# Optimization experiments

Measured on AMD Instinct MI355X. Metric: run time of the kernel, lower is better.

The kernel has to match this reference:

```python
import jax, jax.numpy as jnp
import numpy as np

N_NODES = 150000  # num_users + num_items
EMB_DIM = 64
N_EDGES = 4000000


def setup_inputs() -> dict:
    key = jax.random.key(0)
    k1, k2 = jax.random.split(key)
    x = jax.random.normal(k1, (N_NODES, EMB_DIM), dtype=jnp.float32)
    edge_index = jax.random.randint(k2, (2, N_EDGES), 0, N_NODES, dtype=jnp.int64)
    return {"x": x, "edge_index": edge_index}


def _lgconv(x, row, col, w):
    # message: x[row] * w ; aggregate: scatter-add into col
    msg = x[row] * w[:, None]  # [E, D]
    return jax.ops.segment_sum(msg, col, num_segments=N_NODES)


def reference(x, edge_index):
    row, col = edge_index[0], edge_index[1]
    # gcn_norm without self-loops: deg from target index (col)
    deg = jax.ops.segment_sum(jnp.ones(row.shape[0], x.dtype), col,
                              num_segments=N_NODES)
    dis = jnp.where(deg > 0, jax.lax.rsqrt(jnp.maximum(deg, 1.0)), 0.0)
    w = dis[row] * dis[col]  # [E]

    emb0 = x
    emb1 = _lgconv(emb0, row, col, w)
    emb2 = _lgconv(emb1, row, col, w)
    # stack over layer dim then mean == mean of the three layer embeddings
    out = (emb0 + emb1 + emb2) / 3.0
    return out
```

## Files before the change

### kernel.cpp

```cpp
#include <hip/hip_runtime.h>
#include <hip/hip_bf16.h>


#define EMB_DIM 64
#define BUCKET_BITS 9
#define BUCKET_SZ 512
#define EPB 8192
#define NBMAX 512
#define CAP 16384
#define GSTRIDE 16

typedef float f32x4 __attribute__((ext_vector_type(4)));

__device__ __forceinline__ float bf_lo(unsigned int q) { return __uint_as_float(q << 16); }
__device__ __forceinline__ float bf_hi(unsigned int q) { return __uint_as_float(q & 0xffff0000u); }
__device__ __forceinline__ unsigned int f2bf(float f) {
    unsigned int u = __float_as_uint(f);
    return (u + 0x7fffu + ((u >> 16) & 1u)) >> 16;
}

__global__ void fused_scatter(const int* __restrict__ rows,
                              const int* __restrict__ cols,
                              int* __restrict__ gcur,
                              unsigned int* __restrict__ pairs,
                              int E, int NB) {
    __shared__ unsigned int sbuf[EPB];
    __shared__ unsigned short sbkt[EPB];
    __shared__ int lh[NBMAX];
    __shared__ int lexc[NBMAX];
    __shared__ int ldiff[NBMAX];
    __shared__ int lrank[NBMAX];
    __shared__ int wsum[8];
    int blk = blockIdx.x, t = threadIdx.x;
    for (int b = t; b < NBMAX; b += 1024) lh[b] = 0;
    __syncthreads();
    int start = blk * EPB, end = min(start + EPB, E);
    int nloc = end - start;
    int n4 = nloc >> 2;
    int rem = nloc & 3;
    const int4* c4 = (const int4*)(cols + start);
    const int4* r4 = (const int4*)(rows + start);
    int myc[8], myr[8];
#pragma unroll
    for (int j = 0; j < 8; ++j) myc[j] = -1;
#pragma unroll
    for (int j = 0; j < 2; ++j) {
        int i4 = t + j * 1024;
        if (i4 < n4) {
            int4 cc = c4[i4];
            int4 rr = r4[i4];
            myc[4 * j + 0] = cc.x; myr[4 * j + 0] = rr.x;
            myc[4 * j + 1] = cc.y; myr[4 * j + 1] = rr.y;
            myc[4 * j + 2] = cc.z; myr[4 * j + 2] = rr.z;
            myc[4 * j + 3] = cc.w; myr[4 * j + 3] = rr.w;
        }
    }
    int mycT = -1, myrT = 0;
    if (t < rem) {
        mycT = cols[start + (n4 << 2) + t];
        myrT = rows[start + (n4 << 2) + t];
    }
#pragma unroll
    for (int j = 0; j < 8; ++j)
        if (myc[j] >= 0) atomicAdd(&lh[myc[j] >> BUCKET_BITS], 1);
    if (mycT >= 0) atomicAdd(&lh[mycT >> BUCKET_BITS], 1);
    __syncthreads();
    int v = 0, incl = 0;
    if (t < 512) {
        v = lh[t];
        incl = v;
        int lane = t & 63;
#pragma unroll
        for (int off = 1; off < 64; off <<= 1) {
            int u = __shfl_up(incl, off, 64);
            if (lane >= off) incl += u;
        }
        if (lane == 63) wsum[t >> 6] = incl;
    }
    __syncthreads();
    if (t < 8) {
        int s = wsum[t];
        int inc2 = s;
#pragma unroll
        for (int off = 1; off < 8; off <<= 1) {
            int u = __shfl_up(inc2, off, 64);
            if (t >= off) inc2 += u;
        }
        wsum[t] = inc2 - s;
    }
    __syncthreads();
    int myexc = 0;
    if (t < 512) {
        myexc = (incl - v) + wsum[t >> 6];
        lexc[t] = myexc;
    }
    if (t < NB) {
        int c = lh[t];
        int old = c ? atomicAdd(&gcur[t * GSTRIDE], c) : 0;
        ldiff[t] = (t * CAP + old) - myexc;
        lrank[t] = 0;
    }
    __syncthreads();
#pragma unroll
    for (int j = 0; j < 8; ++j) {
        if (myc[j] >= 0) {
            int b = myc[j] >> BUCKET_BITS;
            int rk = atomicAdd(&lrank[b], 1);
            int p = lexc[b] + rk;
            sbuf[p] = (unsigned)myr[j] |
                      ((unsigned)(myc[j] & (BUCKET_SZ - 1)) << 18);
            sbkt[p] = (unsigned short)b;
        }
    }
    if (mycT >= 0) {
        int b = mycT >> BUCKET_BITS;
        int rk = atomicAdd(&lrank[b], 1);
        int p = lexc[b] + rk;
        sbuf[p] = (unsigned)myrT |
                  ((unsigned)(mycT & (BUCKET_SZ - 1)) << 18);
        sbkt[p] = (unsigned short)b;
    }
    __syncthreads();
    for (int p = t; p < nloc; p += 1024) {
        int b = sbkt[p];
        pairs[ldiff[b] + p] = sbuf[p];
    }
}

__global__ void bucket_finalize(const unsigned int* __restrict__ pairs,
                                const int* __restrict__ gcur,
                                int* __restrict__ edata,
                                int* __restrict__ offsets,
                                float* __restrict__ dis,
                                int N, int E, int NB) {
    __shared__ int sbuf[CAP];
    __shared__ int ccnt[BUCKET_SZ];
    __shared__ int cexc[BUCKET_SZ];
    __shared__ int rnk[BUCKET_SZ];
    __shared__ int wsum[16];
    __shared__ int gb_s;
    int b = blockIdx.x, t = threadIdx.x;
    int pbase = b * CAP;
    int cnt = gcur[b * GSTRIDE];

    int part = 0;
    for (int j = t; j < b; j += 1024) part += gcur[j * GSTRIDE];
#pragma unroll
    for (int off = 32; off; off >>= 1) part += __shfl_down(part, off, 64);
    if ((t & 63) == 0) wsum[t >> 6] = part;
    if (t < BUCKET_SZ) ccnt[t] = 0;
    __syncthreads();
    if (t == 0) {
        int g = 0;
#pragma unroll
        for (int w = 0; w < 16; ++w) g += wsum[w];
        gb_s = g;
    }
    for (int i = t; i < cnt; i += 1024)
        atomicAdd(&ccnt[pairs[pbase + i] >> 18], 1);
    __syncthreads();

    int v = 0, incl = 0;
    if (t < 512) {
        v = ccnt[t];
        incl = v;
        int lane = t & 63;
#pragma unroll
        for (int off = 1; off < 64; off <<= 1) {
            int u = __shfl_up(incl, off, 64);
            if (lane >= off) incl += u;
        }
        if (lane == 63) wsum[t >> 6] = incl;
    }
    __syncthreads();
    if (t < 8) {
        int s = wsum[t];
        int inc2 = s;
#pragma unroll
        for (int off = 1; off < 8; off <<= 1) {
            int u = __shfl_up(inc2, off, 64);
            if (t >= off) inc2 += u;
        }
        wsum[t] = inc2 - s;
    }
    __syncthreads();
    if (t < 512) cexc[t] = (incl - v) + wsum[t >> 6];
    if (t < BUCKET_SZ) rnk[t] = 0;
    __syncthreads();

    int base = gb_s;
    int col0 = b << BUCKET_BITS;
    int ncols = min(BUCKET_SZ, N - col0);
    if (t < ncols) {
        int c = ccnt[t];
        offsets[col0 + t] = base + cexc[t];
        dis[col0 + t] = (c > 0) ? rsqrtf((float)c) : 0.0f;
    }
    __syncthreads();
    for (int i = t; i < cnt; i += 1024) {
        unsigned p = pairs[pbase + i];
        int lc = p >> 18;
        int rk = atomicAdd(&rnk[lc], 1);
        sbuf[cexc[lc] + rk] = p & 0x3FFFF;
    }
    __syncthreads();
    for (int i = t; i < cnt; i += 1024)
        edata[base + i] = sbuf[i];
}

__global__ void yb_kernel(const float* __restrict__ x,
                          const float* __restrict__ dis,
                          unsigned short* __restrict__ yb,
                          int* __restrict__ offsets, int N, int E) {
    int tid = blockIdx.x * blockDim.x + threadIdx.x;
    if (tid == 0) offsets[N] = E;
    int nth = gridDim.x * blockDim.x;
    int total = N * 16;
    for (int u = tid; u < total; u += nth) {
        int lr = u >> 4;
        int part = u & 15;
        float d = dis[lr];
        size_t o = (((size_t)lr) << 6) + part * 4;
        float4 vx = *(const float4*)(x + o);
        uint2 w;
        w.x = f2bf(vx.x * d) | (f2bf(vx.y * d) << 16);
        w.y = f2bf(vx.z * d) | (f2bf(vx.w * d) << 16);
        *(uint2*)(yb + o) = w;
    }
}

__device__ __forceinline__ void acc8(float* acc, uint4 q) {
    acc[0] += bf_lo(q.x);
    acc[1] += bf_hi(q.x);
    acc[2] += bf_lo(q.y);
    acc[3] += bf_hi(q.y);
    acc[4] += bf_lo(q.z);
    acc[5] += bf_hi(q.z);
    acc[6] += bf_lo(q.w);
    acc[7] += bf_hi(q.w);
}

template <bool FINAL>
__global__ void agg_kernel(const unsigned short* __restrict__ embb,
                           const int* __restrict__ edata,
                           const int* __restrict__ offsets,
                           const float* __restrict__ dis,
                           const float* __restrict__ x,
                           unsigned short* __restrict__ outb,
                           float* __restrict__ outf,
                           int n) {
    int wave = (blockIdx.x * blockDim.x + threadIdx.x) >> 6;
    int lane = threadIdx.x & 63;
    int sub = lane >> 3;
    int dest = (wave << 3) + sub;
    if (dest >= n) return;
    int dimo = (lane & 7) * 8;

    int s = offsets[dest];
    int e = offsets[dest + 1];

    float a0[8] = {0, 0, 0, 0, 0, 0, 0, 0};
    float a1[8] = {0, 0, 0, 0, 0, 0, 0, 0};
    const unsigned short* eb = embb + dimo;

    int k = s;
    int kfull = s + ((e - s) & ~7);
    for (; k < kfull; k += 8) {
        int s0 = edata[k];
        int s1 = edata[k + 1];
        int s2 = edata[k + 2];
        int s3 = edata[k + 3];
        int s4 = edata[k + 4];
        int s5 = edata[k + 5];
        int s6 = edata[k + 6];
        int s7 = edata[k + 7];
        uint4 q0 = *(const uint4*)(eb + ((size_t)s0 << 6));
        uint4 q1 = *(const uint4*)(eb + ((size_t)s1 << 6));
        uint4 q2 = *(const uint4*)(eb + ((size_t)s2 << 6));
        uint4 q3 = *(const uint4*)(eb + ((size_t)s3 << 6));
        uint4 q4 = *(const uint4*)(eb + ((size_t)s4 << 6));
        uint4 q5 = *(const uint4*)(eb + ((size_t)s5 << 6));
        uint4 q6 = *(const uint4*)(eb + ((size_t)s6 << 6));
        uint4 q7 = *(const uint4*)(eb + ((size_t)s7 << 6));
        acc8(a0, q0);
        acc8(a1, q1);
        acc8(a0, q2);
        acc8(a1, q3);
        acc8(a0, q4);
        acc8(a1, q5);
        acc8(a0, q6);
        acc8(a1, q7);
    }
    if (k < e) {
        int s0 = edata[k];
        int s1 = (k + 1 < e) ? edata[k + 1] : -1;
        int s2 = (k + 2 < e) ? edata[k + 2] : -1;
        int s3 = (k + 3 < e) ? edata[k + 3] : -1;
        int s4 = (k + 4 < e) ? edata[k + 4] : -1;
        int s5 = (k + 5 < e) ? edata[k + 5] : -1;
        int s6 = (k + 6 < e) ? edata[k + 6] : -1;
        int s7 = (k + 7 < e) ? edata[k + 7] : -1;
        uint4 q0, q1, q2, q3, q4, q5, q6, q7;
        q0 = *(const uint4*)(eb + ((size_t)s0 << 6));
        if (s1 >= 0) q1 = *(const uint4*)(eb + ((size_t)s1 << 6));
        if (s2 >= 0) q2 = *(const uint4*)(eb + ((size_t)s2 << 6));
        if (s3 >= 0) q3 = *(const uint4*)(eb + ((size_t)s3 << 6));
        if (s4 >= 0) q4 = *(const uint4*)(eb + ((size_t)s4 << 6));
        if (s5 >= 0) q5 = *(const uint4*)(eb + ((size_t)s5 << 6));
        if (s6 >= 0) q6 = *(const uint4*)(eb + ((size_t)s6 << 6));
        if (s7 >= 0) q7 = *(const uint4*)(eb + ((size_t)s7 << 6));
        acc8(a0, q0);
        if (s1 >= 0) acc8(a1, q1);
        if (s2 >= 0) acc8(a0, q2);
        if (s3 >= 0) acc8(a1, q3);
        if (s4 >= 0) acc8(a0, q4);
        if (s5 >= 0) acc8(a1, q5);
        if (s6 >= 0) acc8(a0, q6);
        if (s7 >= 0) acc8(a1, q7);
    }

    float acc[8];
#pragma unroll
    for (int j = 0; j < 8; ++j) acc[j] = a0[j] + a1[j];

    float dc = dis[dest];
    size_t o = ((size_t)dest << 6) + dimo;
    if (FINAL) {
        float rd = (dc > 0.0f) ? 1.0f / dc : 0.0f;
        f32x4 xa = __builtin_nontemporal_load((const f32x4*)(x + o));
        f32x4 xc = __builtin_nontemporal_load((const f32x4*)(x + o) + 1);
        uint4 qz = *(const uint4*)(embb + o);
        const float k3 = 1.0f / 3.0f;
        f32x4 r0, r1;
        r0.x = (xa.x + bf_lo(qz.x) * rd + dc * acc[0]) * k3;
        r0.y = (xa.y + bf_hi(qz.x) * rd + dc * acc[1]) * k3;
        r0.z = (xa.z + bf_lo(qz.y) * rd + dc * acc[2]) * k3;
        r0.w = (xa.w + bf_hi(qz.y) * rd + dc * acc[3]) * k3;
        r1.x = (xc.x + bf_lo(qz.z) * rd + dc * acc[4]) * k3;
        r1.y = (xc.y + bf_hi(qz.z) * rd + dc * acc[5]) * k3;
        r1.z = (xc.z + bf_lo(qz.w) * rd + dc * acc[6]) * k3;
        r1.w = (xc.w + bf_hi(qz.w) * rd + dc * acc[7]) * k3;
        __builtin_nontemporal_store(r0, (f32x4*)(outf + o));
        __builtin_nontemporal_store(r1, (f32x4*)(outf + o) + 1);
    } else {
        float zs = dc * dc;
        uint4 q;
        q.x = f2bf(zs * acc[0]) | (f2bf(zs * acc[1]) << 16);
        q.y = f2bf(zs * acc[2]) | (f2bf(zs * acc[3]) << 16);
        q.z = f2bf(zs * acc[4]) | (f2bf(zs * acc[5]) << 16);
        q.w = f2bf(zs * acc[6]) | (f2bf(zs * acc[7]) << 16);
        *(uint4*)(outb + o) = q;
    }
}

extern "C" void kernel_launch(void* const* d_in, const int* in_sizes, int n_in,
                              void* d_out, int out_size, void* d_ws, size_t ws_size,
                              hipStream_t stream) {
    const float* x  = (const float*)d_in[0];
    const int*   ei = (const int*)d_in[1];
    const int E = in_sizes[1] / 2;
    const int N = in_sizes[0] / EMB_DIM;

    const int* rows = ei;
    const int* cols = ei + E;

    const int NB = (N + BUCKET_SZ - 1) >> BUCKET_BITS;
    const int NBLK = (E + EPB - 1) / EPB;

    int*   gcur    = (int*)d_ws;
    float* dis     = (float*)(gcur + 512 * GSTRIDE);
    int*   offsets = (int*)(dis + 150080);
    int*   edata   = offsets + 150080;
    unsigned short* yb = (unsigned short*)(edata + E);
    unsigned short* zb = yb + (size_t)N * EMB_DIM;
    unsigned int* pairs = (unsigned int*)zb;
    float* out = (float*)d_out;

    hipMemsetAsync(gcur, 0, 512 * GSTRIDE * sizeof(int), stream);
    fused_scatter<<<NBLK, 1024, 0, stream>>>(rows, cols, gcur, pairs, E, NB);
    bucket_finalize<<<NB, 1024, 0, stream>>>(pairs, gcur, edata, offsets,
                                             dis, N, E, NB);
    yb_kernel<<<2048, 256, 0, stream>>>(x, dis, yb, offsets, N, E);

    int agg_waves = (N + 7) / 8;
    int agg_blocks = (agg_waves + 3) / 4;
    agg_kernel<false><<<agg_blocks, 256, 0, stream>>>(yb, edata, offsets, dis,
                                                      nullptr, zb, nullptr, N);
    agg_kernel<true><<<agg_blocks, 256, 0, stream>>>(zb, edata, offsets, dis,
                                                     x, nullptr, out, N);
}
```

Baseline: 281.3 us.

## Fuse first aggregation layer into bucket finalize using shared-memory CSR

Degree counting moves into the scatter kernel through global atomics, so the scaled bf16 embeddings can be built before bucket finalization. The bucket finalize kernel then runs the first aggregation layer directly from its shared-memory sorted edge list, which removes one kernel launch and one global read of edata. The pairs buffer now lives in the output buffer, and dis is recomputed from degree counts. The trade-offs are about 4M extra global atomics in the scatter kernel and only 150 blocks of 1024 threads doing the first aggregation, which may cost parallelism.

```diff
diff --git a/kernel.cpp b/kernel.cpp
--- a/kernel.cpp
+++ b/kernel.cpp
@@ -19,9 +19,21 @@
     return (u + 0x7fffu + ((u >> 16) & 1u)) >> 16;
 }
 
+__device__ __forceinline__ void acc8(float* acc, uint4 q) {
+    acc[0] += bf_lo(q.x);
+    acc[1] += bf_hi(q.x);
+    acc[2] += bf_lo(q.y);
+    acc[3] += bf_hi(q.y);
+    acc[4] += bf_lo(q.z);
+    acc[5] += bf_hi(q.z);
+    acc[6] += bf_lo(q.w);
+    acc[7] += bf_hi(q.w);
+}
+
 __global__ void fused_scatter(const int* __restrict__ rows,
                               const int* __restrict__ cols,
                               int* __restrict__ gcur,
+                              int* __restrict__ deg,
                               unsigned int* __restrict__ pairs,
                               int E, int NB) {
     __shared__ unsigned int sbuf[EPB];
@@ -61,9 +73,16 @@
         myrT = rows[start + (n4 << 2) + t];
     }
 #pragma unroll
-    for (int j = 0; j < 8; ++j)
-        if (myc[j] >= 0) atomicAdd(&lh[myc[j] >> BUCKET_BITS], 1);
-    if (mycT >= 0) atomicAdd(&lh[mycT >> BUCKET_BITS], 1);
+    for (int j = 0; j < 8; ++j) {
+        if (myc[j] >= 0) {
+            atomicAdd(&deg[myc[j]], 1);
+            atomicAdd(&lh[myc[j] >> BUCKET_BITS], 1);
+        }
+    }
+    if (mycT >= 0) {
+        atomicAdd(&deg[mycT], 1);
+        atomicAdd(&lh[mycT >> BUCKET_BITS], 1);
+    }
     __syncthreads();
     int v = 0, incl = 0;
     if (t < 512) {
@@ -127,12 +146,36 @@
     }
 }
 
-__global__ void bucket_finalize(const unsigned int* __restrict__ pairs,
-                                const int* __restrict__ gcur,
-                                int* __restrict__ edata,
-                                int* __restrict__ offsets,
-                                float* __restrict__ dis,
-                                int N, int E, int NB) {
+__global__ void yb_kernel(const float* __restrict__ x,
+                          const int* __restrict__ deg,
+                          unsigned short* __restrict__ yb,
+                          int* __restrict__ offsets, int N, int E) {
+    int tid = blockIdx.x * blockDim.x + threadIdx.x;
+    if (tid == 0) offsets[N] = E;
+    int nth = gridDim.x * blockDim.x;
+    int total = N * 16;
+    for (int u = tid; u < total; u += nth) {
+        int lr = u >> 4;
+        int part = u & 15;
+        int dg = deg[lr];
+        float d = (dg > 0) ? rsqrtf((float)dg) : 0.0f;
+        size_t o = (((size_t)lr) << 6) + part * 4;
+        float4 vx = *(const float4*)(x + o);
+        uint2 w;
+        w.x = f2bf(vx.x * d) | (f2bf(vx.y * d) << 16);
+        w.y = f2bf(vx.z * d) | (f2bf(vx.w * d) << 16);
+        *(uint2*)(yb + o) = w;
+    }
+}
+
+__global__ __launch_bounds__(1024)
+void agg1_bucket(const unsigned int* __restrict__ pairs,
+                 const int* __restrict__ gcur,
+                 const unsigned short* __restrict__ yb,
+                 unsigned short* __restrict__ zb,
+                 int* __restrict__ edata,
+                 int* __restrict__ offsets,
+                 int N, int NB) {
     __shared__ int sbuf[CAP];
     __shared__ int ccnt[BUCKET_SZ];
     __shared__ int cexc[BUCKET_SZ];
@@ -184,71 +227,118 @@
         wsum[t] = inc2 - s;
     }
     __syncthreads();
-    if (t < 512) cexc[t] = (incl - v) + wsum[t >> 6];
-    if (t < BUCKET_SZ) rnk[t] = 0;
+    if (t < 512) {
+        int e = (incl - v) + wsum[t >> 6];
+        cexc[t] = e;
+        rnk[t] = e;
+    }
     __syncthreads();
 
     int base = gb_s;
     int col0 = b << BUCKET_BITS;
     int ncols = min(BUCKET_SZ, N - col0);
-    if (t < ncols) {
-        int c = ccnt[t];
-        offsets[col0 + t] = base + cexc[t];
-        dis[col0 + t] = (c > 0) ? rsqrtf((float)c) : 0.0f;
-    }
+    if (t < ncols) offsets[col0 + t] = base + cexc[t];
     __syncthreads();
     for (int i = t; i < cnt; i += 1024) {
         unsigned p = pairs[pbase + i];
         int lc = p >> 18;
         int rk = atomicAdd(&rnk[lc], 1);
-        sbuf[cexc[lc] + rk] = p & 0x3FFFF;
+        sbuf[rk] = p & 0x3FFFF;
     }
     __syncthreads();
     for (int i = t; i < cnt; i += 1024)
         edata[base + i] = sbuf[i];
-}
-
-__global__ void yb_kernel(const float* __restrict__ x,
-                          const float* __restrict__ dis,
-                          unsigned short* __restrict__ yb,
-                          int* __restrict__ offsets, int N, int E) {
-    int tid = blockIdx.x * blockDim.x + threadIdx.x;
-    if (tid == 0) offsets[N] = E;
-    int nth = gridDim.x * blockDim.x;
-    int total = N * 16;
-    for (int u = tid; u < total; u += nth) {
-        int lr = u >> 4;
-        int part = u & 15;
-        float d = dis[lr];
-        size_t o = (((size_t)lr) << 6) + part * 4;
-        float4 vx = *(const float4*)(x + o);
-        uint2 w;
-        w.x = f2bf(vx.x * d) | (f2bf(vx.y * d) << 16);
-        w.y = f2bf(vx.z * d) | (f2bf(vx.w * d) << 16);
-        *(uint2*)(yb + o) = w;
-    }
-}
-
-__device__ __forceinline__ void acc8(float* acc, uint4 q) {
-    acc[0] += bf_lo(q.x);
-    acc[1] += bf_hi(q.x);
-    acc[2] += bf_lo(q.y);
-    acc[3] += bf_hi(q.y);
-    acc[4] += bf_lo(q.z);
-    acc[5] += bf_hi(q.z);
-    acc[6] += bf_lo(q.w);
-    acc[7] += bf_hi(q.w);
-}
-
-template <bool FINAL>
-__global__ void agg_kernel(const unsigned short* __restrict__ embb,
-                           const int* __restrict__ edata,
-                           const int* __restrict__ offsets,
-                           const float* __restrict__ dis,
-                           const float* __restrict__ x,
-                           unsigned short* __restrict__ outb,
-                           float* __restrict__ outf,
-                           int n) {
+
+    int wave = t >> 6;
+    int lane = t & 63;
+    int sub = lane >> 3;
+    int dimo = (lane & 7) * 8;
+    const unsigned short* eb = yb + dimo;
+#pragma unroll 1
+    for (int r = 0; r < 4; ++r) {
+        int dl = (wave << 3) + sub + (r << 7);
+        if (dl >= ncols) break;
+        int cd = ccnt[dl];
+        int s = cexc[dl];
+        int e = s + cd;
+        float a0[8] = {0, 0, 0, 0, 0, 0, 0, 0};
+        float a1[8] = {0, 0, 0, 0, 0, 0, 0, 0};
+        int k = s;
+        int kfull = s + (cd & ~7);
+        for (; k < kfull; k += 8) {
+            int s0 = sbuf[k];
+            int s1 = sbuf[k + 1];
+            int s2 = sbuf[k + 2];
+            int s3 = sbuf[k + 3];
+            int s4 = sbuf[k + 4];
+            int s5 = sbuf[k + 5];
+            int s6 = sbuf[k + 6];
+            int s7 = sbuf[k + 7];
+            uint4 q0 = *(const uint4*)(eb + ((size_t)s0 << 6));
+            uint4 q1 = *(const uint4*)(eb + ((size_t)s1 << 6));
+            uint4 q2 = *(const uint4*)(eb + ((size_t)s2 << 6));
+            uint4 q3 = *(const uint4*)(eb + ((size_t)s3 << 6));
+            uint4 q4 = *(const uint4*)(eb + ((size_t)s4 << 6));
+            uint4 q5 = *(const uint4*)(eb + ((size_t)s5 << 6));
+            uint4 q6 = *(const uint4*)(eb + ((size_t)s6 << 6));
+            uint4 q7 = *(const uint4*)(eb + ((size_t)s7 << 6));
+            acc8(a0, q0);
+            acc8(a1, q1);
+            acc8(a0, q2);
+            acc8(a1, q3);
+            acc8(a0, q4);
+            acc8(a1, q5);
+            acc8(a0, q6);
+            acc8(a1, q7);
+        }
+        if (k < e) {
+            int s0 = sbuf[k];
+            int s1 = (k + 1 < e) ? sbuf[k + 1] : -1;
+            int s2 = (k + 2 < e) ? sbuf[k + 2] : -1;
+            int s3 = (k + 3 < e) ? sbuf[k + 3] : -1;
+            int s4 = (k + 4 < e) ? sbuf[k + 4] : -1;
+            int s5 = (k + 5 < e) ? sbuf[k + 5] : -1;
+            int s6 = (k + 6 < e) ? sbuf[k + 6] : -1;
+            int s7 = (k + 7 < e) ? sbuf[k + 7] : -1;
+            uint4 q0, q1, q2, q3, q4, q5, q6, q7;
+            q0 = *(const uint4*)(eb + ((size_t)s0 << 6));
+            if (s1 >= 0) q1 = *(const uint4*)(eb + ((size_t)s1 << 6));
+            if (s2 >= 0) q2 = *(const uint4*)(eb + ((size_t)s2 << 6));
+            if (s3 >= 0) q3 = *(const uint4*)(eb + ((size_t)s3 << 6));
+            if (s4 >= 0) q4 = *(const uint4*)(eb + ((size_t)s4 << 6));
+            if (s5 >= 0) q5 = *(const uint4*)(eb + ((size_t)s5 << 6));
+            if (s6 >= 0) q6 = *(const uint4*)(eb + ((size_t)s6 << 6));
+            if (s7 >= 0) q7 = *(const uint4*)(eb + ((size_t)s7 << 6));
+            acc8(a0, q0);
+            if (s1 >= 0) acc8(a1, q1);
+            if (s2 >= 0) acc8(a0, q2);
+            if (s3 >= 0) acc8(a1, q3);
+            if (s4 >= 0) acc8(a0, q4);
+            if (s5 >= 0) acc8(a1, q5);
+            if (s6 >= 0) acc8(a0, q6);
+            if (s7 >= 0) acc8(a1, q7);
+        }
+        float acc[8];
+#pragma unroll
+        for (int j = 0; j < 8; ++j) acc[j] = a0[j] + a1[j];
+
+        float dc = (cd > 0) ? rsqrtf((float)cd) : 0.0f;
+        float zs = dc * dc;
+        uint4 q;
+        q.x = f2bf(zs * acc[0]) | (f2bf(zs * acc[1]) << 16);
+        q.y = f2bf(zs * acc[2]) | (f2bf(zs * acc[3]) << 16);
+        q.z = f2bf(zs * acc[4]) | (f2bf(zs * acc[5]) << 16);
+        q.w = f2bf(zs * acc[6]) | (f2bf(zs * acc[7]) << 16);
+        *(uint4*)(zb + (((size_t)(col0 + dl)) << 6) + dimo) = q;
+    }
+}
+
+__global__ void agg2_kernel(const unsigned short* __restrict__ zb,
+                            const int* __restrict__ edata,
+                            const int* __restrict__ offsets,
+                            const float* __restrict__ x,
+                            float* __restrict__ outf,
+                            int n) {
     int wave = (blockIdx.x * blockDim.x + threadIdx.x) >> 6;
     int lane = threadIdx.x & 63;
     int sub = lane >> 3;
@@ -261,7 +351,7 @@
 
     float a0[8] = {0, 0, 0, 0, 0, 0, 0, 0};
     float a1[8] = {0, 0, 0, 0, 0, 0, 0, 0};
-    const unsigned short* eb = embb + dimo;
+    const unsigned short* eb = zb + dimo;
 
     int k = s;
     int kfull = s + ((e - s) & ~7);
@@ -323,34 +413,25 @@
 #pragma unroll
     for (int j = 0; j < 8; ++j) acc[j] = a0[j] + a1[j];
 
-    float dc = dis[dest];
+    int cd = e - s;
+    float dc = (cd > 0) ? rsqrtf((float)cd) : 0.0f;
     size_t o = ((size_t)dest << 6) + dimo;
-    if (FINAL) {
-        float rd = (dc > 0.0f) ? 1.0f / dc : 0.0f;
-        f32x4 xa = __builtin_nontemporal_load((const f32x4*)(x + o));
-        f32x4 xc = __builtin_nontemporal_load((const f32x4*)(x + o) + 1);
-        uint4 qz = *(const uint4*)(embb + o);
-        const float k3 = 1.0f / 3.0f;
-        f32x4 r0, r1;
-        r0.x = (xa.x + bf_lo(qz.x) * rd + dc * acc[0]) * k3;
-        r0.y = (xa.y + bf_hi(qz.x) * rd + dc * acc[1]) * k3;
-        r0.z = (xa.z + bf_lo(qz.y) * rd + dc * acc[2]) * k3;
-        r0.w = (xa.w + bf_hi(qz.y) * rd + dc * acc[3]) * k3;
-        r1.x = (xc.x + bf_lo(qz.z) * rd + dc * acc[4]) * k3;
-        r1.y = (xc.y + bf_hi(qz.z) * rd + dc * acc[5]) * k3;
-        r1.z = (xc.z + bf_lo(qz.w) * rd + dc * acc[6]) * k3;
-        r1.w = (xc.w + bf_hi(qz.w) * rd + dc * acc[7]) * k3;
-        __builtin_nontemporal_store(r0, (f32x4*)(outf + o));
-        __builtin_nontemporal_store(r1, (f32x4*)(outf + o) + 1);
-    } else {
-        float zs = dc * dc;
-        uint4 q;
-        q.x = f2bf(zs * acc[0]) | (f2bf(zs * acc[1]) << 16);
-        q.y = f2bf(zs * acc[2]) | (f2bf(zs * acc[3]) << 16);
-        q.z = f2bf(zs * acc[4]) | (f2bf(zs * acc[5]) << 16);
-        q.w = f2bf(zs * acc[6]) | (f2bf(zs * acc[7]) << 16);
-        *(uint4*)(outb + o) = q;
-    }
+    float rd = (dc > 0.0f) ? 1.0f / dc : 0.0f;
+    f32x4 xa = __builtin_nontemporal_load((const f32x4*)(x + o));
+    f32x4 xc = __builtin_nontemporal_load((const f32x4*)(x + o) + 1);
+    uint4 qz = *(const uint4*)(zb + o);
+    const float k3 = 1.0f / 3.0f;
+    f32x4 r0, r1;
+    r0.x = (xa.x + bf_lo(qz.x) * rd + dc * acc[0]) * k3;
+    r0.y = (xa.y + bf_hi(qz.x) * rd + dc * acc[1]) * k3;
+    r0.z = (xa.z + bf_lo(qz.y) * rd + dc * acc[2]) * k3;
+    r0.w = (xa.w + bf_hi(qz.y) * rd + dc * acc[3]) * k3;
+    r1.x = (xc.x + bf_lo(qz.z) * rd + dc * acc[4]) * k3;
+    r1.y = (xc.y + bf_hi(qz.z) * rd + dc * acc[5]) * k3;
+    r1.z = (xc.z + bf_lo(qz.w) * rd + dc * acc[6]) * k3;
+    r1.w = (xc.w + bf_hi(qz.w) * rd + dc * acc[7]) * k3;
+    __builtin_nontemporal_store(r0, (f32x4*)(outf + o));
+    __builtin_nontemporal_store(r1, (f32x4*)(outf + o) + 1);
 }
 
 extern "C" void kernel_launch(void* const* d_in, const int* in_sizes, int n_in,
@@ -368,24 +449,23 @@
     const int NBLK = (E + EPB - 1) / EPB;
 
     int*   gcur    = (int*)d_ws;
-    float* dis     = (float*)(gcur + 512 * GSTRIDE);
-    int*   offsets = (int*)(dis + 150080);
+    int*   deg     = gcur + 512 * GSTRIDE;
+    int*   offsets = deg + 150080;
     int*   edata   = offsets + 150080;
     unsigned short* yb = (unsigned short*)(edata + E);
     unsigned short* zb = yb + (size_t)N * EMB_DIM;
-    unsigned int* pairs = (unsigned int*)zb;
+    unsigned int* pairs = (unsigned int*)d_out;
     float* out = (float*)d_out;
 
-    hipMemsetAsync(gcur, 0, 512 * GSTRIDE * sizeof(int), stream);
-    fused_scatter<<<NBLK, 1024, 0, stream>>>(rows, cols, gcur, pairs, E, NB);
-    bucket_finalize<<<NB, 1024, 0, stream>>>(pairs, gcur, edata, offsets,
-                                             dis, N, E, NB);
-    yb_kernel<<<2048, 256, 0, stream>>>(x, dis, yb, offsets, N, E);
+    hipMemsetAsync(gcur, 0, (512 * GSTRIDE + 150080) * sizeof(int), stream);
+    fused_scatter<<<NBLK, 1024, 0, stream>>>(rows, cols, gcur, deg, pairs,
+                                             E, NB);
+    yb_kernel<<<2048, 256, 0, stream>>>(x, deg, yb, offsets, N, E);
+    agg1_bucket<<<NB, 1024, 0, stream>>>(pairs, gcur, yb, zb, edata,
+                                         offsets, N, NB);
 
     int agg_waves = (N + 7) / 8;
     int agg_blocks = (agg_waves + 3) / 4;
-    agg_kernel<false><<<agg_blocks, 256, 0, stream>>>(yb, edata, offsets, dis,
-                                                      nullptr, zb, nullptr, N);
-    agg_kernel<true><<<agg_blocks, 256, 0, stream>>>(zb, edata, offsets, dis,
-                                                     x, nullptr, out, N);
-}
+    agg2_kernel<<<agg_blocks, 256, 0, stream>>>(zb, edata, offsets,
+                                                x, out, N);
+}
```

After: 440.2 us. 56.5% more time.
